# Performance work log

Hardware: AMD Instinct MI355X
Metric: run time of the kernel (lower is better)

Reference implementation:

```python
import jax, jax.numpy as jnp
import numpy as np

B = 4_000_000

def setup_inputs() -> dict:
    key = jax.random.key(0)
    x = jax.random.normal(key, (B, 7), dtype=jnp.float32)
    return {"x": x}

def reference(x) -> jnp.ndarray:
    # x: [B, 7] = [qw, qx, qy, qz, tx, ty, tz]
    q0, q1, q2, q3 = x[:, 0], x[:, 1], x[:, 2], x[:, 3]
    t = x[:, 4:7]  # [B, 3]
    q0q0, q1q1, q2q2, q3q3 = q0 * q0, q1 * q1, q2 * q2, q3 * q3
    r00 = q0q0 + q1q1 - q2q2 - q3q3
    r01 = 2.0 * q1 * q2 - 2.0 * q0 * q3
    r02 = 2.0 * q1 * q3 + 2.0 * q0 * q2
    r10 = 2.0 * q1 * q2 + 2.0 * q0 * q3
    r11 = q0q0 - q1q1 + q2q2 - q3q3
    r12 = 2.0 * q2 * q3 - 2.0 * q0 * q1
    r20 = 2.0 * q1 * q3 - 2.0 * q0 * q2
    r21 = 2.0 * q2 * q3 + 2.0 * q0 * q1
    r22 = q0q0 - q1q1 - q2q2 + q3q3
    R = jnp.stack([r00, r01, r02, r10, r11, r12, r20, r21, r22], axis=-1).reshape(-1, 3, 3)
    pose = jnp.concatenate([R, t[:, :, None]], axis=2)  # [B, 3, 4]
    return pose
```

## Files before the change

### kernel.cpp

```cpp
#include <hip/hip_runtime.h>

__global__ __launch_bounds__(256) void quat_pose_kernel(
    const float* __restrict__ x, float* __restrict__ out, int nquad, int B) {
    int i = blockIdx.x * blockDim.x + threadIdx.x;
    if (i >= nquad) return;

    long long row0 = 4ll * i;

    if (row0 + 4 <= (long long)B) {
        const float4* xin = (const float4*)(x + 28ll * i);
        float4 v[7];
#pragma unroll
        for (int k = 0; k < 7; k++) v[k] = xin[k];
        const float* f = (const float*)v;

        float4 o[12];
        float* w4 = (float*)o;
#pragma unroll
        for (int r = 0; r < 4; r++) {
            const float* p = f + 7 * r;
            float q0 = p[0], q1 = p[1], q2 = p[2], q3 = p[3];
            float t0 = p[4], t1 = p[5], t2 = p[6];
            float q00 = q0 * q0, q11 = q1 * q1, q22 = q2 * q2, q33 = q3 * q3;
            float* w = w4 + 12 * r;
            w[0]  = q00 + q11 - q22 - q33;
            w[1]  = 2.0f * (q1 * q2 - q0 * q3);
            w[2]  = 2.0f * (q1 * q3 + q0 * q2);
            w[3]  = t0;
            w[4]  = 2.0f * (q1 * q2 + q0 * q3);
            w[5]  = q00 - q11 + q22 - q33;
            w[6]  = 2.0f * (q2 * q3 - q0 * q1);
            w[7]  = t1;
            w[8]  = 2.0f * (q1 * q3 - q0 * q2);
            w[9]  = 2.0f * (q2 * q3 + q0 * q1);
            w[10] = q00 - q11 - q22 + q33;
            w[11] = t2;
        }
        float4* op = (float4*)(out + 48ll * i);
#pragma unroll
        for (int k = 0; k < 12; k++) op[k] = o[k];
    } else {
        for (long long r = row0; r < (long long)B; ++r) {
            const float* p = x + 7ll * r;
            float q0 = p[0], q1 = p[1], q2 = p[2], q3 = p[3];
            float t0 = p[4], t1 = p[5], t2 = p[6];
            float q00 = q0 * q0, q11 = q1 * q1, q22 = q2 * q2, q33 = q3 * q3;
            float* w = out + 12ll * r;
            w[0]  = q00 + q11 - q22 - q33;
            w[1]  = 2.0f * (q1 * q2 - q0 * q3);
            w[2]  = 2.0f * (q1 * q3 + q0 * q2);
            w[3]  = t0;
            w[4]  = 2.0f * (q1 * q2 + q0 * q3);
            w[5]  = q00 - q11 + q22 - q33;
            w[6]  = 2.0f * (q2 * q3 - q0 * q1);
            w[7]  = t1;
            w[8]  = 2.0f * (q1 * q3 - q0 * q2);
            w[9]  = 2.0f * (q2 * q3 + q0 * q1);
            w[10] = q00 - q11 - q22 + q33;
            w[11] = t2;
        }
    }
}

extern "C" void kernel_launch(void* const* d_in, const int* in_sizes, int n_in,
                              void* d_out, int out_size, void* d_ws, size_t ws_size,
                              hipStream_t stream) {
    const float* x = (const float*)d_in[0];
    float* out = (float*)d_out;
    int B = in_sizes[0] / 7;
    int nquad = (B + 3) / 4;
    int block = 256;
    int grid = (nquad + block - 1) / block;
    quat_pose_kernel<<<grid, block, 0, stream>>>(x, out, nquad, B);
}
```

Measured before the change: 296.4 us.

## Stage input and output through shared memory for coalesced float4 accesses

Each thread previously handled four rows, issuing seven float4 loads and twelve float4 stores at large per-thread strides. Now each block of 256 threads cooperatively loads its contiguous input span into LDS with coalesced float4 reads. Each thread then computes one row into a padded LDS output buffer with a 13-float stride, and the block writes the output back with coalesced float4 stores. The aim is to turn strided global traffic into contiguous wavefront-wide transactions. The cost is two barriers, extra LDS traffic, and possibly misaligned 16-byte LDS reads caused by the 13-float row stride.

```diff
diff --git a/kernel.cpp b/kernel.cpp
--- a/kernel.cpp
+++ b/kernel.cpp
@@ -1,51 +1,42 @@
 #include <hip/hip_runtime.h>
 
+
 __global__ __launch_bounds__(256) void quat_pose_kernel(
-    const float* __restrict__ x, float* __restrict__ out, int nquad, int B) {
-    int i = blockIdx.x * blockDim.x + threadIdx.x;
-    if (i >= nquad) return;
+    const float* __restrict__ x, float* __restrict__ out, int B) {
+    __shared__ float s_in[1792];
+    __shared__ float s_out[256 * 13];
 
-    long long row0 = 4ll * i;
+    const int t = threadIdx.x;
+    const int b = blockIdx.x;
+    const long long rowBase = 256ll * b;
 
-    if (row0 + 4 <= (long long)B) {
-        const float4* xin = (const float4*)(x + 28ll * i);
-        float4 v[7];
-#pragma unroll
-        for (int k = 0; k < 7; k++) v[k] = xin[k];
-        const float* f = (const float*)v;
+    const long long inF4Base = 448ll * b;
+    const long long totalInF4 = (7ll * B) / 4;
+    {
+        const float4* xin4 = (const float4*)x;
+        long long i0 = inF4Base + t;
+        if (i0 < totalInF4) {
+            float4 v = xin4[i0];
+            ((float4*)s_in)[t] = v;
+        }
+        if (t < 192) {
+            long long i1 = inF4Base + 256 + t;
+            if (i1 < totalInF4) {
+                float4 v = xin4[i1];
+                ((float4*)s_in)[256 + t] = v;
+            }
+        }
+    }
+    __syncthreads();
 
-        float4 o[12];
-        float* w4 = (float*)o;
-#pragma unroll
-        for (int r = 0; r < 4; r++) {
-            const float* p = f + 7 * r;
+    {
+        const long long r = rowBase + t;
+        if (r < (long long)B) {
+            const float* p = s_in + 7 * t;
             float q0 = p[0], q1 = p[1], q2 = p[2], q3 = p[3];
             float t0 = p[4], t1 = p[5], t2 = p[6];
             float q00 = q0 * q0, q11 = q1 * q1, q22 = q2 * q2, q33 = q3 * q3;
-            float* w = w4 + 12 * r;
-            w[0]  = q00 + q11 - q22 - q33;
-            w[1]  = 2.0f * (q1 * q2 - q0 * q3);
-            w[2]  = 2.0f * (q1 * q3 + q0 * q2);
-            w[3]  = t0;
-            w[4]  = 2.0f * (q1 * q2 + q0 * q3);
-            w[5]  = q00 - q11 + q22 - q33;
-            w[6]  = 2.0f * (q2 * q3 - q0 * q1);
-            w[7]  = t1;
-            w[8]  = 2.0f * (q1 * q3 - q0 * q2);
-            w[9]  = 2.0f * (q2 * q3 + q0 * q1);
-            w[10] = q00 - q11 - q22 + q33;
-            w[11] = t2;
-        }
-        float4* op = (float4*)(out + 48ll * i);
-#pragma unroll
-        for (int k = 0; k < 12; k++) op[k] = o[k];
-    } else {
-        for (long long r = row0; r < (long long)B; ++r) {
-            const float* p = x + 7ll * r;
-            float q0 = p[0], q1 = p[1], q2 = p[2], q3 = p[3];
-            float t0 = p[4], t1 = p[5], t2 = p[6];
-            float q00 = q0 * q0, q11 = q1 * q1, q22 = q2 * q2, q33 = q3 * q3;
-            float* w = out + 12ll * r;
+            float* w = s_out + 13 * t;
             w[0]  = q00 + q11 - q22 - q33;
             w[1]  = 2.0f * (q1 * q2 - q0 * q3);
             w[2]  = 2.0f * (q1 * q3 + q0 * q2);
@@ -60,6 +51,24 @@
             w[11] = t2;
         }
     }
+    __syncthreads();
+
+    {
+        const long long outF4Base = 768ll * b;
+        const long long totalOutF4 = 3ll * B;
+        float4* out4 = (float4*)out;
+#pragma unroll
+        for (int k = 0; k < 3; k++) {
+            int m = t + 256 * k;
+            long long gm = outF4Base + m;
+            if (gm < totalOutF4) {
+                int row = m / 3;
+                int off = 4 * (m % 3);
+                float4 v = *(const float4*)(s_out + 13 * row + off);
+                out4[gm] = v;
+            }
+        }
+    }
 }
 
 extern "C" void kernel_launch(void* const* d_in, const int* in_sizes, int n_in,
@@ -68,8 +77,6 @@
     const float* x = (const float*)d_in[0];
     float* out = (float*)d_out;
     int B = in_sizes[0] / 7;
-    int nquad = (B + 3) / 4;
-    int block = 256;
-    int grid = (nquad + block - 1) / block;
-    quat_pose_kernel<<<grid, block, 0, stream>>>(x, out, nquad, B);
+    int grid = (B + 255) / 256;
+    quat_pose_kernel<<<grid, 256, 0, stream>>>(x, out, B);
 }
```

Result: faster. 270.1 us (-8.9%).
